# Kernel optimization log

Hardware: AMD Instinct MI355X
Metric: run time of the kernel (lower is better)

The kernel has to match this reference:

```python
import jax, jax.numpy as jnp
import numpy as np

D_MODEL = 768
NUM_HEADS = 12
D_K = D_MODEL // NUM_HEADS


def setup_inputs() -> dict:
    key = jax.random.key(0)
    ks = jax.random.split(key, 12)
    B, S = 4, 2048
    s = 1.0 / np.sqrt(D_MODEL)
    inp = {
        "query": jax.random.normal(ks[0], (B, S, D_MODEL), jnp.float32),
        "key": jax.random.normal(ks[1], (B, S, D_MODEL), jnp.float32),
        "value": jax.random.normal(ks[2], (B, S, D_MODEL), jnp.float32),
        "Wq": jax.random.normal(ks[3], (D_MODEL, D_MODEL), jnp.float32) * s,
        "bq": jnp.zeros((D_MODEL,), jnp.float32),
        "Wk": jax.random.normal(ks[4], (D_MODEL, D_MODEL), jnp.float32) * s,
        "bk": jnp.zeros((D_MODEL,), jnp.float32),
        "Wv": jax.random.normal(ks[5], (D_MODEL, D_MODEL), jnp.float32) * s,
        "bv": jnp.zeros((D_MODEL,), jnp.float32),
        "Wo": jax.random.normal(ks[6], (D_MODEL, D_MODEL), jnp.float32) * s,
        "bo": jnp.zeros((D_MODEL,), jnp.float32),
    }
    return inp


def _split_heads(x):
    B, S, _ = x.shape
    return x.reshape(B, S, NUM_HEADS, D_K).transpose(0, 2, 1, 3)  # [B,H,S,Dk]


def reference(query, key, value, Wq, bq, Wk, bk, Wv, bv, Wo, bo):
    # Linear projections (torch nn.Linear: x @ W.T + b)
    Q = _split_heads(query @ Wq.T + bq)
    K = _split_heads(key @ Wk.T + bk)
    V = _split_heads(value @ Wv.T + bv)
    scale = 1.0 / jnp.sqrt(jnp.asarray(D_K, Q.dtype))
    scores = jnp.einsum("bhqd,bhkd->bhqk", Q, K) * scale  # [B,H,S,S]
    attn = jax.nn.softmax(scores, axis=-1)
    # dropout is identity in eval mode
    out = jnp.einsum("bhqk,bhkd->bhqd", attn, V)  # [B,H,S,Dk]
    B, H, S, Dk = out.shape
    out = out.transpose(0, 2, 1, 3).reshape(B, S, H * Dk)
    return out @ Wo.T + bo
```

## Files before the change

kernel.cpp:

```cpp
#include <hip/hip_runtime.h>
#include <hip/hip_bf16.h>

typedef _Float16 half8 __attribute__((ext_vector_type(8)));
typedef _Float16 h4 __attribute__((ext_vector_type(4)));
typedef __fp16 fp16x2 __attribute__((ext_vector_type(2)));
typedef float f32x4 __attribute__((ext_vector_type(4)));

#define D_MODEL 768
#define NUM_HEADS 12
#define D_K 64
#define SEQ 2048
#define BATCH 4
#define M_TOTAL (BATCH * SEQ)
#define W_ELEMS (D_MODEL * D_MODEL)
#define X_ELEMS (M_TOTAL * D_MODEL)
#define QSCALE 0.18033688011112042f
#define SOFF 4.0f

__device__ __forceinline__ void gll16(const _Float16* g, _Float16* l) {
    __builtin_amdgcn_global_load_lds(
        (const __attribute__((address_space(1))) unsigned int*)g,
        (__attribute__((address_space(3))) unsigned int*)l,
        16, 0, 0);
}

__global__ void convert_all(
    const float* __restrict__ w0, const float* __restrict__ w1,
    const float* __restrict__ w2, const float* __restrict__ w3,
    const float* __restrict__ x0, const float* __restrict__ x1,
    const float* __restrict__ x2, _Float16* __restrict__ dst)
{
    const size_t W8 = W_ELEMS / 8, X8 = X_ELEMS / 8;
    size_t i = (size_t)blockIdx.x * blockDim.x + threadIdx.x;
    const float* src;
    size_t off;
    if (i < 4 * W8) {
        size_t slab = i / W8;
        off = i - slab * W8;
        src = (slab == 0) ? w0 : (slab == 1) ? w1 : (slab == 2) ? w2 : w3;
    } else {
        size_t j = i - 4 * W8;
        size_t slab = j / X8;
        off = j - slab * X8;
        src = (slab == 0) ? x0 : (slab == 1) ? x1 : x2;
    }
    float4 f0 = ((const float4*)src)[off * 2];
    float4 f1 = ((const float4*)src)[off * 2 + 1];
    half8 h;
    h[0] = (_Float16)f0.x; h[1] = (_Float16)f0.y;
    h[2] = (_Float16)f0.z; h[3] = (_Float16)f0.w;
    h[4] = (_Float16)f1.x; h[5] = (_Float16)f1.y;
    h[6] = (_Float16)f1.z; h[7] = (_Float16)f1.w;
    ((half8*)dst)[i] = h;
}

__global__ __launch_bounds__(256) void gemm_qkv(
    const _Float16* __restrict__ Xall, const _Float16* __restrict__ Wall,
    const float* __restrict__ bq, const float* __restrict__ bk, const float* __restrict__ bv,
    _Float16* __restrict__ Qo, _Float16* __restrict__ Ko, _Float16* __restrict__ Vto)
{
    __shared__ __align__(16) char smem[36864];
    _Float16* As = (_Float16*)smem;
    _Float16* Bs = As + 128 * 64;

    const int lid = blockIdx.x + (int)gridDim.x * (blockIdx.y + (int)gridDim.y * blockIdx.z);
    const int xcd = lid & 7, idx = lid >> 3;
    const int mloc = idx / 18, rr = idx - mloc * 18;
    const int z = rr / 6, nn = rr - (rr / 6) * 6;
    const int m0 = (xcd * 8 + mloc) * 128;
    const int n0 = nn * 128;

    const _Float16* X = Xall + (size_t)z * X_ELEMS;
    const _Float16* W = Wall + (size_t)z * W_ELEMS;

    const int t = threadIdx.x;
    const int w = t >> 6;
    const int l = t & 63;
    const int ln = t & 15;
    const int quad = (t >> 4) & 3;
    const int wm = w >> 1, wn = w & 1;

    const int srow = l >> 3;
    const int scol = (l & 7) ^ srow;

    f32x4 acc[4][4] = {};

    for (int k0 = 0; k0 < D_MODEL; k0 += 64) {
#pragma unroll
        for (int jj = 0; jj < 4; ++jj) {
            int j = w * 4 + jj;
            int row = j * 8 + srow;
            gll16(X + (size_t)(m0 + row) * D_MODEL + k0 + scol * 8, As + j * 512);
            gll16(W + (size_t)(n0 + row) * D_MODEL + k0 + scol * 8, Bs + j * 512);
        }
        __syncthreads();

#pragma unroll
        for (int kk = 0; kk < 2; ++kk) {
            half8 a[4], b[4];
#pragma unroll
            for (int i = 0; i < 4; ++i) {
                int ra = wm * 64 + i * 16 + ln;
                int rb = wn * 64 + i * 16 + ln;
                a[i] = *(const half8*)&As[ra * 64 + (((kk * 4 + quad) ^ (ln & 7)) * 8)];
                b[i] = *(const half8*)&Bs[rb * 64 + (((kk * 4 + quad) ^ (ln & 7)) * 8)];
            }
            if (z <= 1) {
#pragma unroll
                for (int i = 0; i < 4; ++i)
#pragma unroll
                    for (int j2 = 0; j2 < 4; ++j2)
                        acc[i][j2] = __builtin_amdgcn_mfma_f32_16x16x32_f16(b[j2], a[i], acc[i][j2], 0, 0, 0);
            } else {
#pragma unroll
                for (int i = 0; i < 4; ++i)
#pragma unroll
                    for (int j2 = 0; j2 < 4; ++j2)
                        acc[i][j2] = __builtin_amdgcn_mfma_f32_16x16x32_f16(a[i], b[j2], acc[i][j2], 0, 0, 0);
            }
        }
        __syncthreads();
    }

    if (z <= 1) {
        const float* bias = (z == 0) ? bq : bk;
        _Float16* dst = (z == 0) ? Qo : Ko;
        const int head = (n0 + wn * 64) >> 6;
#pragma unroll
        for (int i = 0; i < 4; ++i) {
            int m = m0 + wm * 64 + i * 16 + ln;
            int b_ = m >> 11, s_ = m & 2047;
            _Float16* rowp = dst + ((size_t)((b_ * NUM_HEADS + head) * SEQ + s_)) * D_K;
#pragma unroll
            for (int j = 0; j < 4; ++j) {
                int dbase = j * 16 + quad * 4;
                f32x4 bn = *(const f32x4*)&bias[n0 + wn * 64 + dbase];
                h4 o;
#pragma unroll
                for (int r = 0; r < 4; ++r) {
                    float v = acc[i][j][r] + bn[r];
                    if (z == 0) v *= QSCALE;
                    o[r] = (_Float16)v;
                }
                *(h4*)&rowp[dbase] = o;
            }
        }
    } else {
        const float* bias = bv;
        _Float16* T = (_Float16*)smem + (size_t)w * (64 * 72);
#pragma unroll
        for (int i = 0; i < 4; ++i) {
#pragma unroll
            for (int j = 0; j < 4; ++j) {
                float bn = bias[n0 + wn * 64 + j * 16 + ln];
                h4 hh;
#pragma unroll
                for (int r = 0; r < 4; ++r) hh[r] = (_Float16)(acc[i][j][r] + bn);
                *(h4*)&T[(j * 16 + ln) * 72 + i * 16 + quad * 4] = hh;
            }
        }
        const int b_ = m0 >> 11;
        const int s0 = (m0 & 2047) + wm * 64;
        const int head = (n0 >> 6) + wn;
        _Float16* base = Vto + (size_t)(b_ * NUM_HEADS + head) * D_K * SEQ + s0;
        const int p = l & 7, tt = p >> 2, qq = p & 3;
#pragma unroll
        for (int r8 = 0; r8 < 8; ++r8) {
            int nl = r8 * 8 + (l >> 3);
            h4 lo = *(const h4*)&T[nl * 72 + tt * 32 + qq * 4];
            h4 hi = *(const h4*)&T[nl * 72 + tt * 32 + 16 + qq * 4];
            half8 v = __builtin_shufflevector(lo, hi, 0, 1, 2, 3, 4, 5, 6, 7);
            *(half8*)(base + (size_t)nl * SEQ + p * 8) = v;
        }
    }
}

__global__ __launch_bounds__(256, 3) void attn(
    const _Float16* __restrict__ Qg, const _Float16* __restrict__ Kg,
    const _Float16* __restrict__ Vtg, _Float16* __restrict__ ctx)
{
    __shared__ __align__(16) _Float16 Ks[2][64 * 64];
    __shared__ __align__(16) _Float16 Vs[2][64 * 64];

    const int t = threadIdx.x;
    const int w = t >> 6;
    const int l = t & 63;
    const int ln = t & 15;
    const int quad = (t >> 4) & 3;

    const int lid = blockIdx.x + (int)gridDim.x * blockIdx.y;
    const int nid = (lid & 7) * ((SEQ / 128) * (BATCH * NUM_HEADS) / 8) + (lid >> 3);
    const int bh = nid >> 4;
    const int q0 = (nid & 15) * 128 + w * 32;

    const _Float16* Qh = Qg + (size_t)bh * SEQ * D_K;
    const _Float16* Kh = Kg + (size_t)bh * SEQ * D_K;
    const _Float16* Vh = Vtg + (size_t)bh * D_K * SEQ;

    const int srow = l >> 3;
    const int scol = (l & 7) ^ srow;
    const _Float16* Ksrc0 = Kh + (size_t)(w * 16 + srow) * D_K + scol * 8;
    const _Float16* Ksrc1 = Kh + (size_t)(w * 16 + 8 + srow) * D_K + scol * 8;
    const _Float16* Vsrc0 = Vh + (size_t)(w * 16 + srow) * SEQ + scol * 8;
    const _Float16* Vsrc1 = Vh + (size_t)(w * 16 + 8 + srow) * SEQ + scol * 8;

    half8 qf[2][2];
#pragma unroll
    for (int qt = 0; qt < 2; ++qt)
#pragma unroll
        for (int dh = 0; dh < 2; ++dh)
            qf[qt][dh] = *(const half8*)(Qh + (size_t)(q0 + qt * 16 + ln) * D_K + dh * 32 + quad * 8);

    f32x4 acc[2][4] = {};
    f32x4 lsum[2] = {};
    f32x4 S[2][4];
    h4 pB[2][4];

    const int c0 = (quad ^ (ln & 7)) * 8;
    const int c1 = ((4 + quad) ^ (ln & 7)) * 8;

    auto stageK = [&](int c, int B) {
        const size_t koff = (size_t)c * 64 * D_K;
        gll16(Ksrc0 + koff, &Ks[B][w * 1024]);
        gll16(Ksrc1 + koff, &Ks[B][w * 1024 + 512]);
    };
    auto stageV = [&](int c, int B) {
        const size_t voff = (size_t)c * 64;
        gll16(Vsrc0 + voff, &Vs[B][w * 1024]);
        gll16(Vsrc1 + voff, &Vs[B][w * 1024 + 512]);
    };

    auto qk = [&](int B) {
        const _Float16* Ksc = Ks[B];
#pragma unroll
        for (int kt = 0; kt < 4; ++kt) {
            half8 kf0 = *(const half8*)&Ksc[(kt * 16 + ln) * 64 + c0];
            half8 kf1 = *(const half8*)&Ksc[(kt * 16 + ln) * 64 + c1];
#pragma unroll
            for (int qt = 0; qt < 2; ++qt) {
                f32x4 s = {-SOFF, -SOFF, -SOFF, -SOFF};
                s = __builtin_amdgcn_mfma_f32_16x16x32_f16(kf0, qf[qt][0], s, 0, 0, 0);
                s = __builtin_amdgcn_mfma_f32_16x16x32_f16(kf1, qf[qt][1], s, 0, 0, 0);
                S[qt][kt] = s;
            }
        }
    };

    auto smx = [&]() {
#pragma unroll
        for (int qt = 0; qt < 2; ++qt)
#pragma unroll
            for (int kt = 0; kt < 4; ++kt) {
                f32x4 s = S[qt][kt];
                f32x4 p;
                p[0] = __builtin_amdgcn_exp2f(s[0]);
                p[1] = __builtin_amdgcn_exp2f(s[1]);
                p[2] = __builtin_amdgcn_exp2f(s[2]);
                p[3] = __builtin_amdgcn_exp2f(s[3]);
                lsum[qt] += p;
                fp16x2 r0 = __builtin_amdgcn_cvt_pkrtz(p[0], p[1]);
                fp16x2 r1 = __builtin_amdgcn_cvt_pkrtz(p[2], p[3]);
                h4 h;
                h[0] = (_Float16)r0[0]; h[1] = (_Float16)r0[1];
                h[2] = (_Float16)r1[0]; h[3] = (_Float16)r1[1];
                pB[qt][kt] = h;
            }
    };

    auto pv = [&](int B) {
        const _Float16* Vsc = Vs[B];
        half8 pA0 = __builtin_shufflevector(pB[0][0], pB[0][1], 0, 1, 2, 3, 4, 5, 6, 7);
        half8 pA1 = __builtin_shufflevector(pB[0][2], pB[0][3], 0, 1, 2, 3, 4, 5, 6, 7);
        half8 pC0 = __builtin_shufflevector(pB[1][0], pB[1][1], 0, 1, 2, 3, 4, 5, 6, 7);
        half8 pC1 = __builtin_shufflevector(pB[1][2], pB[1][3], 0, 1, 2, 3, 4, 5, 6, 7);
        __builtin_amdgcn_s_setprio(1);
#pragma unroll
        for (int dt = 0; dt < 4; ++dt) {
            half8 va = *(const half8*)&Vsc[(dt * 16 + ln) * 64 + c0];
            half8 vb = *(const half8*)&Vsc[(dt * 16 + ln) * 64 + c1];
            acc[0][dt] = __builtin_amdgcn_mfma_f32_16x16x32_f16(va, pA0, acc[0][dt], 0, 0, 0);
            acc[0][dt] = __builtin_amdgcn_mfma_f32_16x16x32_f16(vb, pA1, acc[0][dt], 0, 0, 0);
            acc[1][dt] = __builtin_amdgcn_mfma_f32_16x16x32_f16(va, pC0, acc[1][dt], 0, 0, 0);
            acc[1][dt] = __builtin_amdgcn_mfma_f32_16x16x32_f16(vb, pC1, acc[1][dt], 0, 0, 0);
        }
        __builtin_amdgcn_s_setprio(0);
    };

    stageK(0, 0);
    stageK(1, 1);
    stageV(0, 0);
    asm volatile("s_waitcnt vmcnt(0)" ::: "memory");
    __builtin_amdgcn_s_barrier();
    qk(0);

    for (int c = 0; c < 31; ++c) {
        asm volatile("s_waitcnt vmcnt(0)" ::: "memory");
        __builtin_amdgcn_s_barrier();
        if (c < 30) stageK(c + 2, c & 1);
        stageV(c + 1, (c + 1) & 1);
        smx();
        qk((c + 1) & 1);
        pv(c & 1);
    }
    asm volatile("s_waitcnt vmcnt(0)" ::: "memory");
    __builtin_amdgcn_s_barrier();
    smx();
    pv(1);

    const int h = bh % NUM_HEADS, b = bh / NUM_HEADS;
#pragma unroll
    for (int qt = 0; qt < 2; ++qt) {
        float lp = lsum[qt][0] + lsum[qt][1] + lsum[qt][2] + lsum[qt][3];
        lp += __shfl_xor(lp, 16);
        lp += __shfl_xor(lp, 32);
        float rinv = __builtin_amdgcn_rcpf(lp);
        int q = q0 + qt * 16 + ln;
#pragma unroll
        for (int dt = 0; dt < 4; ++dt) {
            h4 o;
            o[0] = (_Float16)(acc[qt][dt][0] * rinv);
            o[1] = (_Float16)(acc[qt][dt][1] * rinv);
            o[2] = (_Float16)(acc[qt][dt][2] * rinv);
            o[3] = (_Float16)(acc[qt][dt][3] * rinv);
            *(h4*)&ctx[((size_t)(b * SEQ + q)) * D_MODEL + h * D_K + dt * 16 + quad * 4] = o;
        }
    }
}

__global__ __launch_bounds__(256) void gemm_out(
    const _Float16* __restrict__ A, const _Float16* __restrict__ W,
    const float* __restrict__ bo, float* __restrict__ out)
{
    __shared__ __align__(16) _Float16 As[128 * 64];
    __shared__ __align__(16) _Float16 Bs[64 * 64];

    const int t = threadIdx.x;
    const int w = t >> 6;
    const int l = t & 63;
    const int ln = t & 15;
    const int quad = (t >> 4) & 3;
    const int wm = w >> 1, wn = w & 1;

    const int lid = blockIdx.x + (int)gridDim.x * blockIdx.y;
    const int xcd = lid & 7, idx = lid >> 3;
    const int mloc = idx / 12, nn = idx - mloc * 12;
    const int m0 = (xcd * 8 + mloc) * 128;
    const int n0 = nn * 64;

    const int srow = l >> 3;
    const int scol = (l & 7) ^ srow;

    f32x4 acc[4][2] = {};

    for (int k0 = 0; k0 < D_MODEL; k0 += 64) {
#pragma unroll
        for (int jj = 0; jj < 4; ++jj) {
            int j = w * 4 + jj;
            int row = j * 8 + srow;
            gll16(A + (size_t)(m0 + row) * D_MODEL + k0 + scol * 8, As + j * 512);
        }
#pragma unroll
        for (int jj = 0; jj < 2; ++jj) {
            int j = w * 2 + jj;
            int row = j * 8 + srow;
            gll16(W + (size_t)(n0 + row) * D_MODEL + k0 + scol * 8, Bs + j * 512);
        }
        __syncthreads();

#pragma unroll
        for (int kk = 0; kk < 2; ++kk) {
            half8 a[4], b[2];
#pragma unroll
            for (int i = 0; i < 4; ++i) {
                int ra = wm * 64 + i * 16 + ln;
                a[i] = *(const half8*)&As[ra * 64 + (((kk * 4 + quad) ^ (ln & 7)) * 8)];
            }
#pragma unroll
            for (int i = 0; i < 2; ++i) {
                int rb = wn * 32 + i * 16 + ln;
                b[i] = *(const half8*)&Bs[rb * 64 + (((kk * 4 + quad) ^ (ln & 7)) * 8)];
            }
#pragma unroll
            for (int i = 0; i < 4; ++i)
#pragma unroll
                for (int j2 = 0; j2 < 2; ++j2)
                    acc[i][j2] = __builtin_amdgcn_mfma_f32_16x16x32_f16(b[j2], a[i], acc[i][j2], 0, 0, 0);
        }
        __syncthreads();
    }

#pragma unroll
    for (int i = 0; i < 4; ++i) {
        int m = m0 + wm * 64 + i * 16 + ln;
        float* rowp = out + (size_t)m * D_MODEL;
#pragma unroll
        for (int j = 0; j < 2; ++j) {
            int nb = n0 + wn * 32 + j * 16 + quad * 4;
            f32x4 o = acc[i][j] + *(const f32x4*)&bo[nb];
            *(f32x4*)&rowp[nb] = o;
        }
    }
}

extern "C" void kernel_launch(void* const* d_in, const int* in_sizes, int n_in,
                              void* d_out, int out_size, void* d_ws, size_t ws_size,
                              hipStream_t stream) {
    const float* query = (const float*)d_in[0];
    const float* key   = (const float*)d_in[1];
    const float* value = (const float*)d_in[2];
    const float* Wq = (const float*)d_in[3];
    const float* bq = (const float*)d_in[4];
    const float* Wk = (const float*)d_in[5];
    const float* bk = (const float*)d_in[6];
    const float* Wv = (const float*)d_in[7];
    const float* bv = (const float*)d_in[8];
    const float* Wo = (const float*)d_in[9];
    const float* bo = (const float*)d_in[10];
    float* out = (float*)d_out;

    _Float16* ws = (_Float16*)d_ws;
    _Float16* Wb  = ws;
    _Float16* Xb  = Wb + 4 * (size_t)W_ELEMS;
    _Float16* Qb  = Xb + 3 * (size_t)X_ELEMS;
    _Float16* Kb  = Qb + (size_t)X_ELEMS;
    _Float16* Vtb = Kb + (size_t)X_ELEMS;
    _Float16* ctx = Vtb + (size_t)X_ELEMS;

    const size_t total8 = (4 * (size_t)W_ELEMS + 3 * (size_t)X_ELEMS) / 8;
    convert_all<<<(int)(total8 / 256), 256, 0, stream>>>(
        Wq, Wk, Wv, Wo, query, key, value, Wb);

    gemm_qkv<<<dim3(M_TOTAL / 128, D_MODEL / 128, 3), 256, 0, stream>>>(
        Xb, Wb, bq, bk, bv, Qb, Kb, Vtb);

    attn<<<dim3(SEQ / 128, BATCH * NUM_HEADS), 256, 0, stream>>>(Qb, Kb, Vtb, ctx);

    gemm_out<<<dim3(M_TOTAL / 128, D_MODEL / 64), 256, 0, stream>>>(
        ctx, Wb + 3 * (size_t)W_ELEMS, bo, out);
}
```

Baseline: 258.7 us.

## Triple-buffer QKV GEMM with 256x128 tiles and 512-thread blocks

Rewrites the QKV projection GEMM to use 512-thread blocks covering 256x128 output tiles, with a three-stage LDS ring buffer. Global-to-LDS loads for tile k+2 are issued between the fragment reads and the MFMAs of tile k, using explicit vmcnt waits, raw barriers and setprio around the MFMA bursts. The aim is to hide load latency and halve B-tile refetches per output, at the cost of more LDS use (about 144KB per block) and lower occupancy. The grid is flattened to 1D with an XCD-aware mapping.

```diff
diff --git a/kernel.cpp b/kernel.cpp
--- a/kernel.cpp
+++ b/kernel.cpp
@@ -54,20 +54,19 @@
     ((half8*)dst)[i] = h;
 }
 
-__global__ __launch_bounds__(256) void gemm_qkv(
+__global__ __launch_bounds__(512, 2) void gemm_qkv(
     const _Float16* __restrict__ Xall, const _Float16* __restrict__ Wall,
     const float* __restrict__ bq, const float* __restrict__ bk, const float* __restrict__ bv,
     _Float16* __restrict__ Qo, _Float16* __restrict__ Ko, _Float16* __restrict__ Vto)
 {
-    __shared__ __align__(16) char smem[36864];
-    _Float16* As = (_Float16*)smem;
-    _Float16* Bs = As + 128 * 64;
-
-    const int lid = blockIdx.x + (int)gridDim.x * (blockIdx.y + (int)gridDim.y * blockIdx.z);
+    __shared__ __align__(16) _Float16 smemA[3 * 256 * 64];
+    __shared__ __align__(16) _Float16 smemB[3 * 128 * 64];
+
+    const int lid = blockIdx.x;
     const int xcd = lid & 7, idx = lid >> 3;
     const int mloc = idx / 18, rr = idx - mloc * 18;
     const int z = rr / 6, nn = rr - (rr / 6) * 6;
-    const int m0 = (xcd * 8 + mloc) * 128;
+    const int m0 = (xcd * 4 + mloc) * 256;
     const int n0 = nn * 128;
 
     const _Float16* X = Xall + (size_t)z * X_ELEMS;
@@ -85,16 +84,33 @@
 
     f32x4 acc[4][4] = {};
 
-    for (int k0 = 0; k0 < D_MODEL; k0 += 64) {
-#pragma unroll
-        for (int jj = 0; jj < 4; ++jj) {
-            int j = w * 4 + jj;
-            int row = j * 8 + srow;
-            gll16(X + (size_t)(m0 + row) * D_MODEL + k0 + scol * 8, As + j * 512);
-            gll16(W + (size_t)(n0 + row) * D_MODEL + k0 + scol * 8, Bs + j * 512);
-        }
-        __syncthreads();
-
+    auto stageH0 = [&](int k, int B) {
+        const int k0 = k * 64;
+        _Float16* Ad = smemA + B * (256 * 64);
+#pragma unroll
+        for (int ja = 0; ja < 3; ++ja) {
+            int row = m0 + ja * 64 + w * 8 + srow;
+            gll16(X + (size_t)row * D_MODEL + k0 + scol * 8, Ad + ja * 4096 + w * 512);
+        }
+    };
+    auto stageH1 = [&](int k, int B) {
+        const int k0 = k * 64;
+        _Float16* Ad = smemA + B * (256 * 64);
+        _Float16* Bd = smemB + B * (128 * 64);
+        {
+            int row = m0 + 192 + w * 8 + srow;
+            gll16(X + (size_t)row * D_MODEL + k0 + scol * 8, Ad + 3 * 4096 + w * 512);
+        }
+#pragma unroll
+        for (int jb = 0; jb < 2; ++jb) {
+            int row = n0 + jb * 64 + w * 8 + srow;
+            gll16(W + (size_t)row * D_MODEL + k0 + scol * 8, Bd + jb * 4096 + w * 512);
+        }
+    };
+
+    auto computeK = [&](int B, bool doStage, int k2, int B2) {
+        const _Float16* Asb = smemA + B * (256 * 64);
+        const _Float16* Bsb = smemB + B * (128 * 64);
 #pragma unroll
         for (int kk = 0; kk < 2; ++kk) {
             half8 a[4], b[4];
@@ -102,9 +118,12 @@
             for (int i = 0; i < 4; ++i) {
                 int ra = wm * 64 + i * 16 + ln;
                 int rb = wn * 64 + i * 16 + ln;
-                a[i] = *(const half8*)&As[ra * 64 + (((kk * 4 + quad) ^ (ln & 7)) * 8)];
-                b[i] = *(const half8*)&Bs[rb * 64 + (((kk * 4 + quad) ^ (ln & 7)) * 8)];
-            }
+                a[i] = *(const half8*)&Asb[ra * 64 + (((kk * 4 + quad) ^ (ln & 7)) * 8)];
+                b[i] = *(const half8*)&Bsb[rb * 64 + (((kk * 4 + quad) ^ (ln & 7)) * 8)];
+            }
+            if (doStage) { if (kk == 0) stageH0(k2, B2); else stageH1(k2, B2); }
+            __builtin_amdgcn_s_barrier();
+            __builtin_amdgcn_s_setprio(1);
             if (z <= 1) {
 #pragma unroll
                 for (int i = 0; i < 4; ++i)
@@ -118,9 +137,25 @@
                     for (int j2 = 0; j2 < 4; ++j2)
                         acc[i][j2] = __builtin_amdgcn_mfma_f32_16x16x32_f16(a[i], b[j2], acc[i][j2], 0, 0, 0);
             }
-        }
-        __syncthreads();
-    }
+            __builtin_amdgcn_s_setprio(0);
+            __builtin_amdgcn_s_barrier();
+        }
+    };
+
+    stageH0(0, 0); stageH1(0, 0);
+    stageH0(1, 1); stageH1(1, 1);
+
+    for (int k = 0; k < 10; ++k) {
+        asm volatile("s_waitcnt vmcnt(6)" ::: "memory");
+        __builtin_amdgcn_s_barrier();
+        computeK(k % 3, true, k + 2, (k + 2) % 3);
+    }
+    asm volatile("s_waitcnt vmcnt(6)" ::: "memory");
+    __builtin_amdgcn_s_barrier();
+    computeK(1, false, 0, 0);
+    asm volatile("s_waitcnt vmcnt(0)" ::: "memory");
+    __builtin_amdgcn_s_barrier();
+    computeK(2, false, 0, 0);
 
     if (z <= 1) {
         const float* bias = (z == 0) ? bq : bk;
@@ -147,7 +182,7 @@
         }
     } else {
         const float* bias = bv;
-        _Float16* T = (_Float16*)smem + (size_t)w * (64 * 72);
+        _Float16* T = smemA + (size_t)w * (64 * 72);
 #pragma unroll
         for (int i = 0; i < 4; ++i) {
 #pragma unroll
@@ -430,7 +465,7 @@
     convert_all<<<(int)(total8 / 256), 256, 0, stream>>>(
         Wq, Wk, Wv, Wo, query, key, value, Wb);
 
-    gemm_qkv<<<dim3(M_TOTAL / 128, D_MODEL / 128, 3), 256, 0, stream>>>(
+    gemm_qkv<<<dim3((M_TOTAL / 256) * (D_MODEL / 128) * 3), 512, 0, stream>>>(
         Xb, Wb, bq, bk, bv, Qb, Kb, Vtb);
 
     attn<<<dim3(SEQ / 128, BATCH * NUM_HEADS), 256, 0, stream>>>(Qb, Kb, Vtb, ctx);
```

Measured after the change: 253.7 us. Within noise of the previous version (-2.0%).
